# Kernel optimization log

Measured on AMD Instinct MI355X. Metric: run time of the kernel, lower is better.

The kernel has to match this reference:

```python
import jax, jax.numpy as jnp
import numpy as np

N = 100000   # num_nodes
E = 1250000  # num_edges
IN = 64
HID = 64
OUT = 64
LN_EPS = 1e-5


def _gcn_conv(x, src, dst, W, b, n):
    # PyG GCNConv: add self-loops, symmetric deg^{-1/2} normalization, then linear.
    h = x @ W  # (N, out)
    deg = jax.ops.segment_sum(jnp.ones(src.shape[0], h.dtype), dst, num_segments=n) + 1.0  # +1 self-loop
    dinv = jax.lax.rsqrt(deg)
    norm = dinv[src] * dinv[dst]  # (E,)
    out = jax.ops.segment_sum(h[src] * norm[:, None], dst, num_segments=n)
    out = out + h * (dinv * dinv)[:, None]  # self-loop message
    return out + b


def _sage_conv(x, src, dst, Wl, bl, Wr, n):
    # PyG SAGEConv(aggr='mean'): lin_l(mean_{j in N(i)} x_j) + lin_r(x_i); bias only in lin_l.
    cnt = jax.ops.segment_sum(jnp.ones(src.shape[0], x.dtype), dst, num_segments=n)
    agg = jax.ops.segment_sum(x[src], dst, num_segments=n) / jnp.maximum(cnt, 1.0)[:, None]
    return agg @ Wl + bl + x @ Wr


def _layer_norm(x, g, b):
    mu = jnp.mean(x, axis=-1, keepdims=True)
    var = jnp.var(x, axis=-1, keepdims=True)
    return (x - mu) * jax.lax.rsqrt(var + LN_EPS) * g + b


def setup_inputs() -> dict:
    key = jax.random.key(0)
    ks = jax.random.split(key, 16)
    def w(k, shape):
        fan_in = shape[0]
        return (jax.random.normal(k, shape, jnp.float32) / np.sqrt(fan_in)).astype(jnp.float32)
    x = jax.random.normal(ks[0], (N, IN), jnp.float32)
    edge_index = jax.random.randint(ks[1], (2, E), 0, N, dtype=jnp.int64)
    return {
        "x": x,
        "edge_index": edge_index,
        "gcn_w1": w(ks[2], (IN, HID)), "gcn_b1": jnp.zeros((HID,), jnp.float32),
        "gcn_w2": w(ks[3], (HID, OUT)), "gcn_b2": jnp.zeros((OUT,), jnp.float32),
        "sage_wl1": w(ks[4], (IN, HID)), "sage_bl1": jnp.zeros((HID,), jnp.float32),
        "sage_wr1": w(ks[5], (IN, HID)),
        "sage_wl2": w(ks[6], (HID, OUT)), "sage_bl2": jnp.zeros((OUT,), jnp.float32),
        "sage_wr2": w(ks[7], (HID, OUT)),
        "gcn_ln_g": jnp.ones((OUT,), jnp.float32), "gcn_ln_b": jnp.zeros((OUT,), jnp.float32),
        "sage_ln_g": jnp.ones((OUT,), jnp.float32), "sage_ln_b": jnp.zeros((OUT,), jnp.float32),
        "proj_w": w(ks[8], (2 * OUT, OUT)), "proj_b": jnp.zeros((OUT,), jnp.float32),
    }


def reference(x, edge_index, gcn_w1, gcn_b1, gcn_w2, gcn_b2,
              sage_wl1, sage_bl1, sage_wr1, sage_wl2, sage_bl2, sage_wr2,
              gcn_ln_g, gcn_ln_b, sage_ln_g, sage_ln_b, proj_w, proj_b):
    src, dst = edge_index[0], edge_index[1]
    n = x.shape[0]
    # GCN branch (dropout p=0 / eval -> identity)
    g = jax.nn.relu(_gcn_conv(x, src, dst, gcn_w1, gcn_b1, n))
    g = _gcn_conv(g, src, dst, gcn_w2, gcn_b2, n)
    # SAGE branch
    s = jax.nn.relu(_sage_conv(x, src, dst, sage_wl1, sage_bl1, sage_wr1, n))
    s = _sage_conv(s, src, dst, sage_wl2, sage_bl2, sage_wr2, n)
    # Norm + projected-concat fusion
    g = _layer_norm(g, gcn_ln_g, gcn_ln_b)
    s = _layer_norm(s, sage_ln_g, sage_ln_b)
    cat = jnp.concatenate([g, s], axis=-1)  # (N, 2*OUT)
    return cat @ proj_w + proj_b
```

## Files before the change

### kernel.cpp

```cpp
#include <hip/hip_runtime.h>


#define SCAN_CHUNK 2048

typedef __attribute__((ext_vector_type(8))) short short8;
typedef __attribute__((ext_vector_type(4))) short short4v;
typedef __attribute__((ext_vector_type(4))) float floatx4;

__device__ __forceinline__ unsigned short f2bf(float f) {
    unsigned int u = __float_as_uint(f);
    unsigned int r = u + 0x7FFFu + ((u >> 16) & 1u);
    return (unsigned short)(r >> 16);
}
__device__ __forceinline__ float bf2f(unsigned short h) {
    return __uint_as_float(((unsigned int)h) << 16);
}

__device__ __forceinline__ unsigned lds_addr(const void* p) {
    return (unsigned)(unsigned long long)(__attribute__((address_space(3))) const char*)p;
}

__device__ __forceinline__ short8 cat44(short4v lo, short4v hi) {
    short8 r;
    r[0] = lo[0]; r[1] = lo[1]; r[2] = lo[2]; r[3] = lo[3];
    r[4] = hi[0]; r[5] = hi[1]; r[6] = hi[2]; r[7] = hi[3];
    return r;
}

template<int NF, int CTB>
__device__ __forceinline__ void tr_read4(unsigned a0, short8 bf[4]) {
    short4v l0, h0, l1, h1, l2, h2, l3, h3;
    asm volatile(
        "ds_read_b64_tr_b16 %0, %8 offset:%9\n\t"
        "ds_read_b64_tr_b16 %1, %8 offset:%10\n\t"
        "ds_read_b64_tr_b16 %2, %8 offset:%11\n\t"
        "ds_read_b64_tr_b16 %3, %8 offset:%12\n\t"
        "ds_read_b64_tr_b16 %4, %8 offset:%13\n\t"
        "ds_read_b64_tr_b16 %5, %8 offset:%14\n\t"
        "ds_read_b64_tr_b16 %6, %8 offset:%15\n\t"
        "ds_read_b64_tr_b16 %7, %8 offset:%16\n\t"
        "s_waitcnt lgkmcnt(0)"
        : "=&v"(l0), "=&v"(h0), "=&v"(l1), "=&v"(h1),
          "=&v"(l2), "=&v"(h2), "=&v"(l3), "=&v"(h3)
        : "v"(a0),
          "i"((0 * NF + CTB + 0) * 128), "i"((1 * NF + CTB + 0) * 128),
          "i"((0 * NF + CTB + 1) * 128), "i"((1 * NF + CTB + 1) * 128),
          "i"((0 * NF + CTB + 2) * 128), "i"((1 * NF + CTB + 2) * 128),
          "i"((0 * NF + CTB + 3) * 128), "i"((1 * NF + CTB + 3) * 128)
        : "memory");
    bf[0] = cat44(l0, h0);
    bf[1] = cat44(l1, h1);
    bf[2] = cat44(l2, h2);
    bf[3] = cat44(l3, h3);
}

__global__ void k_count(const int* __restrict__ ei, int E, int* __restrict__ cnt,
                        int* __restrict__ rank) {
    int i = blockIdx.x * blockDim.x + threadIdx.x;
    int e = i * 4;
    if (e + 4 <= E) {
        int4 d = *(const int4*)&ei[E + e];
        int4 r;
        r.x = atomicAdd(&cnt[d.x], 1);
        r.y = atomicAdd(&cnt[d.y], 1);
        r.z = atomicAdd(&cnt[d.z], 1);
        r.w = atomicAdd(&cnt[d.w], 1);
        *(int4*)&rank[e] = r;
    } else {
        for (int j = e; j < E; ++j) rank[j] = atomicAdd(&cnt[ei[E + j]], 1);
    }
}

__global__ void k_scan_reduce(const int* __restrict__ cnt, int N, int* __restrict__ blockSums) {
    __shared__ int lds[256];
    int base = blockIdx.x * SCAN_CHUNK;
    int t = threadIdx.x;
    int s = 0;
    for (int j = 0; j < 8; ++j) {
        int idx = base + t * 8 + j;
        if (idx < N) s += cnt[idx];
    }
    lds[t] = s;
    __syncthreads();
    for (int d = 128; d > 0; d >>= 1) {
        if (t < d) lds[t] += lds[t + d];
        __syncthreads();
    }
    if (t == 0) blockSums[blockIdx.x] = lds[0];
}

__global__ void k_scan_spine(int* __restrict__ blockSums, int B) {
    if (threadIdx.x == 0 && blockIdx.x == 0) {
        int run = 0;
        for (int b = 0; b < B; ++b) { int v = blockSums[b]; blockSums[b] = run; run += v; }
    }
}

__global__ void k_scan_write(const int* __restrict__ cnt, int N,
                             const int* __restrict__ blockSums,
                             int* __restrict__ offs, float* __restrict__ dinv) {
    __shared__ int lds[256];
    int base = blockIdx.x * SCAN_CHUNK;
    int t = threadIdx.x;
    int v[8];
    int s = 0;
    for (int j = 0; j < 8; ++j) {
        int idx = base + t * 8 + j;
        v[j] = (idx < N) ? cnt[idx] : 0;
        s += v[j];
    }
    lds[t] = s;
    __syncthreads();
    for (int d = 1; d < 256; d <<= 1) {
        int x = (t >= d) ? lds[t - d] : 0;
        __syncthreads();
        lds[t] += x;
        __syncthreads();
    }
    int excl = (t == 0) ? 0 : lds[t - 1];
    int run = blockSums[blockIdx.x] + excl;
    for (int j = 0; j < 8; ++j) {
        int idx = base + t * 8 + j;
        if (idx < N) {
            offs[idx] = run;
            run += v[j];
            dinv[idx] = rsqrtf((float)v[j] + 1.0f);
            if (idx == N - 1) offs[N] = run;
        }
    }
}

__global__ void k_fill(const int* __restrict__ ei, int E, const int* __restrict__ offs,
                       const int* __restrict__ rank, const float* __restrict__ dinv,
                       int* __restrict__ csr, unsigned int* __restrict__ pk, int use_pk) {
    int i = blockIdx.x * blockDim.x + threadIdx.x;
    int e = i * 4;
    if (e + 4 <= E) {
        int4 s = *(const int4*)&ei[e];
        int4 d = *(const int4*)&ei[E + e];
        int4 r = *(const int4*)&rank[e];
        int p0 = offs[d.x] + r.x, p1 = offs[d.y] + r.y;
        int p2 = offs[d.z] + r.z, p3 = offs[d.w] + r.w;
        csr[p0] = s.x; csr[p1] = s.y; csr[p2] = s.z; csr[p3] = s.w;
        if (use_pk) {
            pk[p0] = ((unsigned)(d.x & 15) << 16) | f2bf(dinv[s.x] * dinv[d.x]);
            pk[p1] = ((unsigned)(d.y & 15) << 16) | f2bf(dinv[s.y] * dinv[d.y]);
            pk[p2] = ((unsigned)(d.z & 15) << 16) | f2bf(dinv[s.z] * dinv[d.z]);
            pk[p3] = ((unsigned)(d.w & 15) << 16) | f2bf(dinv[s.w] * dinv[d.w]);
        }
    } else {
        for (int j = e; j < E; ++j) {
            int dd = ei[E + j];
            int p = offs[dd] + rank[j];
            csr[p] = ei[j];
            if (use_pk) pk[p] = ((unsigned)(dd & 15) << 16) | f2bf(dinv[ei[j]] * dinv[dd]);
        }
    }
}

__global__ void k_xtobf16(const float* __restrict__ x, unsigned short* __restrict__ xb, int total) {
    int i = blockIdx.x * blockDim.x + threadIdx.x;
    int e = i * 8;
    if (e + 8 <= total) {
        float4 a = *(const float4*)&x[e];
        float4 b = *(const float4*)&x[e + 4];
        short8 o;
        o[0] = (short)f2bf(a.x); o[1] = (short)f2bf(a.y);
        o[2] = (short)f2bf(a.z); o[3] = (short)f2bf(a.w);
        o[4] = (short)f2bf(b.x); o[5] = (short)f2bf(b.y);
        o[6] = (short)f2bf(b.z); o[7] = (short)f2bf(b.w);
        *(short8*)&xb[e] = o;
    } else {
        for (int j = e; j < total; ++j) xb[j] = f2bf(x[j]);
    }
}

template<int ROWSH>
__launch_bounds__(256)
__global__ void k_gatherM(const unsigned short* __restrict__ feat,
                          const int* __restrict__ csr,
                          const unsigned int* __restrict__ pk,
                          const int* __restrict__ offs, const int* __restrict__ cnt,
                          const float* __restrict__ dinv,
                          unsigned short* __restrict__ agg, int N) {
    constexpr int NF = ROWSH / 16;
    constexpr int LPR = ROWSH / 8;
    constexpr int EPP = 64 / LPR;
    constexpr int PASSES = 32 / EPP;

    __shared__ unsigned short sbuf[4 * 32 * ROWSH];

    const int lane = threadIdx.x & 63;
    const int wave = threadIdx.x >> 6;
    const int base = blockIdx.x * 64 + wave * 16;
    if (base >= N) return;

    unsigned short* wb = &sbuf[wave * 32 * ROWSH];
    const unsigned wboff = lds_addr(wb);
    const int q = lane >> 4;
    const int d16 = lane & 15;

    const int se = lane / LPR;
    const int sf = (lane % LPR) * 8;
    const int sf_sub = sf >> 4;
    const int sf_lo = sf & 15;

    const int elo = offs[base];
    const int ehi = offs[min(base + 16, N)];

    floatx4 accg[4], accs[4];
#pragma unroll
    for (int i = 0; i < 4; ++i) {
        accg[i] = floatx4{0.f, 0.f, 0.f, 0.f};
        accs[i] = floatx4{0.f, 0.f, 0.f, 0.f};
    }

    const unsigned a0 = wboff + (unsigned)(q * 2 * NF) * 128u + (unsigned)d16 * 8u;

    for (int k0 = elo; k0 < ehi; k0 += 32) {
        short8 stg[PASSES];
#pragma unroll
        for (int p = 0; p < PASSES; ++p) {
            int idx = k0 + p * EPP + se;
            int src = csr[idx < ehi ? idx : ehi - 1];
            stg[p] = *(const short8*)&feat[(size_t)src * ROWSH + sf];
        }
        int i0 = k0 + q * 8;
        short8 aG, aS;
#pragma unroll
        for (int j = 0; j < 8; ++j) {
            unsigned u = pk[i0 + j];
            bool ok = ((int)(u >> 16) == d16) && (i0 + j < ehi);
            aG[j] = ok ? (short)(u & 0xffffu) : (short)0;
            aS[j] = ok ? (short)0x3F80 : (short)0;
        }
#pragma unroll
        for (int p = 0; p < PASSES; ++p) {
            int e = p * EPP + se;
            int elem = ((e >> 2) * NF + sf_sub) * 64 + (e & 3) * 16 + sf_lo;
            *(short8*)&wb[elem] = stg[p];
        }
        asm volatile("s_waitcnt lgkmcnt(0)" ::: "memory");
        __builtin_amdgcn_sched_barrier(0);

        short8 bG[4];
        tr_read4<NF, 0>(a0, bG);
#pragma unroll
        for (int ct = 0; ct < 4; ++ct)
            accg[ct] = __builtin_amdgcn_mfma_f32_16x16x32_bf16(aG, bG[ct], accg[ct], 0, 0, 0);
        if constexpr (NF == 8) {
            short8 bS[4];
            tr_read4<NF, 4>(a0, bS);
#pragma unroll
            for (int ct = 0; ct < 4; ++ct)
                accs[ct] = __builtin_amdgcn_mfma_f32_16x16x32_bf16(aS, bS[ct], accs[ct], 0, 0, 0);
        } else {
#pragma unroll
            for (int ct = 0; ct < 4; ++ct)
                accs[ct] = __builtin_amdgcn_mfma_f32_16x16x32_bf16(aS, bG[ct], accs[ct], 0, 0, 0);
        }
    }

    {
        short8 stg[PASSES];
#pragma unroll
        for (int p = 0; p < PASSES; ++p) {
            int nd = base + p * EPP + se;
            if (nd >= N) nd = N - 1;
            stg[p] = *(const short8*)&feat[(size_t)nd * ROWSH + sf];
        }
        float ds = dinv[min(base + d16, N - 1)];
        unsigned short wself = f2bf(ds * ds);
        short8 aG;
#pragma unroll
        for (int j = 0; j < 8; ++j) {
            bool ok = ((q * 8 + j) == d16) && (base + d16 < N);
            aG[j] = ok ? (short)wself : (short)0;
        }
#pragma unroll
        for (int p = 0; p < PASSES; ++p) {
            int e = p * EPP + se;
            int elem = ((e >> 2) * NF + sf_sub) * 64 + (e & 3) * 16 + sf_lo;
            *(short8*)&wb[elem] = stg[p];
        }
        asm volatile("s_waitcnt lgkmcnt(0)" ::: "memory");
        __builtin_amdgcn_sched_barrier(0);
        short8 bG[4];
        tr_read4<NF, 0>(a0, bG);
#pragma unroll
        for (int ct = 0; ct < 4; ++ct)
            accg[ct] = __builtin_amdgcn_mfma_f32_16x16x32_bf16(aG, bG[ct], accg[ct], 0, 0, 0);
    }

#pragma unroll
    for (int r = 0; r < 4; ++r) {
        int node = base + q * 4 + r;
        if (node < N) {
            float rn = 1.0f / fmaxf((float)cnt[node], 1.0f);
#pragma unroll
            for (int ct = 0; ct < 4; ++ct) {
                agg[(size_t)node * 128 + ct * 16 + d16]      = f2bf(accg[ct][r]);
                agg[(size_t)node * 128 + 64 + ct * 16 + d16] = f2bf(accs[ct][r] * rn);
            }
        }
    }
}

__device__ __forceinline__ void xor_reduce8(float4& a, float4& b) {
    a.x += __shfl_xor(a.x, 16, 64); a.y += __shfl_xor(a.y, 16, 64);
    a.z += __shfl_xor(a.z, 16, 64); a.w += __shfl_xor(a.w, 16, 64);
    b.x += __shfl_xor(b.x, 16, 64); b.y += __shfl_xor(b.y, 16, 64);
    b.z += __shfl_xor(b.z, 16, 64); b.w += __shfl_xor(b.w, 16, 64);
    a.x += __shfl_xor(a.x, 32, 64); a.y += __shfl_xor(a.y, 32, 64);
    a.z += __shfl_xor(a.z, 32, 64); a.w += __shfl_xor(a.w, 32, 64);
    b.x += __shfl_xor(b.x, 32, 64); b.y += __shfl_xor(b.y, 32, 64);
    b.z += __shfl_xor(b.z, 32, 64); b.w += __shfl_xor(b.w, 32, 64);
}

__device__ __forceinline__ float red16(float v) {
    v += __shfl_xor(v, 1, 64);
    v += __shfl_xor(v, 2, 64);
    v += __shfl_xor(v, 4, 64);
    v += __shfl_xor(v, 8, 64);
    return v;
}

__global__ void k_gather1_f32(const float* __restrict__ x, const int* __restrict__ csr,
                              const int* __restrict__ offs, const int* __restrict__ cnt,
                              const float* __restrict__ dinv,
                              unsigned short* __restrict__ agg, int N) {
    int lane = threadIdx.x & 63;
    int wave = threadIdx.x >> 6;
    int node = blockIdx.x * 4 + wave;
    if (node >= N) return;
    int c = lane & 15, grp = lane >> 4;

    int st = offs[node];
    int cn = cnt[node];
    float di = dinv[node];

    float4 aA = {0.f, 0.f, 0.f, 0.f}, aB = {0.f, 0.f, 0.f, 0.f};
    for (int e = 0; e < cn; e += 8) {
        int i0 = e + grp, i1 = e + 4 + grp;
        float m0 = (i0 < cn) ? 1.f : 0.f;
        float m1 = (i1 < cn) ? 1.f : 0.f;
        int s0 = csr[st + (i0 < cn ? i0 : cn - 1)];
        int s1 = csr[st + (i1 < cn ? i1 : cn - 1)];
        float w0 = m0 * dinv[s0];
        float w1 = m1 * dinv[s1];
        float4 v0 = *(const float4*)&x[(size_t)s0 * 64 + 4 * c];
        float4 v1 = *(const float4*)&x[(size_t)s1 * 64 + 4 * c];
        aA.x += w0 * v0.x + w1 * v1.x; aA.y += w0 * v0.y + w1 * v1.y;
        aA.z += w0 * v0.z + w1 * v1.z; aA.w += w0 * v0.w + w1 * v1.w;
        aB.x += m0 * v0.x + m1 * v1.x; aB.y += m0 * v0.y + m1 * v1.y;
        aB.z += m0 * v0.z + m1 * v1.z; aB.w += m0 * v0.w + m1 * v1.w;
    }
    xor_reduce8(aA, aB);

    if (grp == 0) {
        float4 sq = *(const float4*)&x[(size_t)node * 64 + 4 * c];
        float d2 = di * di;
        ushort4 o;
        o.x = f2bf(di * aA.x + d2 * sq.x); o.y = f2bf(di * aA.y + d2 * sq.y);
        o.z = f2bf(di * aA.z + d2 * sq.z); o.w = f2bf(di * aA.w + d2 * sq.w);
        *(ushort4*)&agg[(size_t)node * 128 + 4 * c] = o;
    } else if (grp == 1) {
        float rn = 1.0f / fmaxf((float)cn, 1.0f);
        ushort4 o;
        o.x = f2bf(aB.x * rn); o.y = f2bf(aB.y * rn);
        o.z = f2bf(aB.z * rn); o.w = f2bf(aB.w * rn);
        *(ushort4*)&agg[(size_t)node * 128 + 64 + 4 * c] = o;
    }
}

__global__ void k_gather2(const unsigned short* __restrict__ gs, const int* __restrict__ csr,
                          const int* __restrict__ offs, const int* __restrict__ cnt,
                          const float* __restrict__ dinv,
                          unsigned short* __restrict__ agg, int N) {
    int lane = threadIdx.x & 63;
    int wave = threadIdx.x >> 6;
    int node = blockIdx.x * 4 + wave;
    if (node >= N) return;
    int c = lane & 15, grp = lane >> 4;

    int st = offs[node];
    int cn = cnt[node];
    float di = dinv[node];

    float4 aC = {0.f, 0.f, 0.f, 0.f}, aD = {0.f, 0.f, 0.f, 0.f};
    for (int e = 0; e < cn; e += 8) {
        int i0 = e + grp, i1 = e + 4 + grp;
        float m0 = (i0 < cn) ? 1.f : 0.f;
        float m1 = (i1 < cn) ? 1.f : 0.f;
        int s0 = csr[st + (i0 < cn ? i0 : cn - 1)];
        int s1 = csr[st + (i1 < cn ? i1 : cn - 1)];
        float w0 = m0 * dinv[s0];
        float w1 = m1 * dinv[s1];
        const unsigned short* p0 = gs + (size_t)s0 * 128 + 4 * c;
        const unsigned short* p1 = gs + (size_t)s1 * 128 + 4 * c;
        ushort4 g0u = *(const ushort4*)p0;
        ushort4 g1u = *(const ushort4*)p1;
        ushort4 t0u = *(const ushort4*)(p0 + 64);
        ushort4 t1u = *(const ushort4*)(p1 + 64);
        aC.x += w0 * bf2f(g0u.x) + w1 * bf2f(g1u.x);
        aC.y += w0 * bf2f(g0u.y) + w1 * bf2f(g1u.y);
        aC.z += w0 * bf2f(g0u.z) + w1 * bf2f(g1u.z);
        aC.w += w0 * bf2f(g0u.w) + w1 * bf2f(g1u.w);
        aD.x += m0 * bf2f(t0u.x) + m1 * bf2f(t1u.x);
        aD.y += m0 * bf2f(t0u.y) + m1 * bf2f(t1u.y);
        aD.z += m0 * bf2f(t0u.z) + m1 * bf2f(t1u.z);
        aD.w += m0 * bf2f(t0u.w) + m1 * bf2f(t1u.w);
    }
    xor_reduce8(aC, aD);

    if (grp == 0) {
        ushort4 su = *(const ushort4*)&gs[(size_t)node * 128 + 4 * c];
        float d2 = di * di;
        ushort4 o;
        o.x = f2bf(di * aC.x + d2 * bf2f(su.x));
        o.y = f2bf(di * aC.y + d2 * bf2f(su.y));
        o.z = f2bf(di * aC.z + d2 * bf2f(su.z));
        o.w = f2bf(di * aC.w + d2 * bf2f(su.w));
        *(ushort4*)&agg[(size_t)node * 128 + 4 * c] = o;
    } else if (grp == 1) {
        float rn = 1.0f / fmaxf((float)cn, 1.0f);
        ushort4 o;
        o.x = f2bf(aD.x * rn); o.y = f2bf(aD.y * rn);
        o.z = f2bf(aD.z * rn); o.w = f2bf(aD.w * rn);
        *(ushort4*)&agg[(size_t)node * 128 + 64 + 4 * c] = o;
    }
}

__launch_bounds__(512, 1)
__global__ void k_gemm1(const unsigned short* __restrict__ agg,
                        const unsigned short* __restrict__ xb,
                        const float* __restrict__ xf, int use_xb,
                        const float* __restrict__ W1, const float* __restrict__ b1,
                        const float* __restrict__ Wl1, const float* __restrict__ bl1,
                        const float* __restrict__ Wr1,
                        unsigned short* __restrict__ buf1, int N) {
    alignas(16) __shared__ unsigned short sW[3][4096];
    int t = threadIdx.x;
    for (int i = t; i < 1536; i += 512) {
        int m = i >> 9;
        int rem = i & 511;
        int f = rem >> 6;
        int L = rem & 63;
        int kb = (f >> 2) * 32 + (L >> 4) * 8;
        int o = (f & 3) * 16 + (L & 15);
        const float* Wsrc = (m == 0) ? W1 : (m == 1) ? Wl1 : Wr1;
        unsigned short* dst = &sW[m][f * 512 + L * 8];
        #pragma unroll
        for (int j = 0; j < 8; ++j) dst[j] = f2bf(Wsrc[(kb + j) * 64 + o]);
    }
    __syncthreads();

    int lane = t & 63;
    int wave = t >> 6;
    int quad = lane >> 4;
    int n16 = lane & 15;
    int base = blockIdx.x * 128 + wave * 16;
    if (base >= N) return;

    int nm = base + n16;
    if (nm >= N) nm = N - 1;
    const unsigned short* ar = agg + (size_t)nm * 128;

    {
        short8 a0 = *(const short8*)(ar + quad * 8);
        short8 a1 = *(const short8*)(ar + 32 + quad * 8);
        floatx4 g0 = {0.f, 0.f, 0.f, 0.f}, g1 = g0, g2 = g0, g3 = g0;
        g0 = __builtin_amdgcn_mfma_f32_16x16x32_bf16(a0, *(const short8*)&sW[0][0 * 512 + lane * 8], g0, 0, 0, 0);
        g0 = __builtin_amdgcn_mfma_f32_16x16x32_bf16(a1, *(const short8*)&sW[0][4 * 512 + lane * 8], g0, 0, 0, 0);
        g1 = __builtin_amdgcn_mfma_f32_16x16x32_bf16(a0, *(const short8*)&sW[0][1 * 512 + lane * 8], g1, 0, 0, 0);
        g1 = __builtin_amdgcn_mfma_f32_16x16x32_bf16(a1, *(const short8*)&sW[0][5 * 512 + lane * 8], g1, 0, 0, 0);
        g2 = __builtin_amdgcn_mfma_f32_16x16x32_bf16(a0, *(const short8*)&sW[0][2 * 512 + lane * 8], g2, 0, 0, 0);
        g2 = __builtin_amdgcn_mfma_f32_16x16x32_bf16(a1, *(const short8*)&sW[0][6 * 512 + lane * 8], g2, 0, 0, 0);
        g3 = __builtin_amdgcn_mfma_f32_16x16x32_bf16(a0, *(const short8*)&sW[0][3 * 512 + lane * 8], g3, 0, 0, 0);
        g3 = __builtin_amdgcn_mfma_f32_16x16x32_bf16(a1, *(const short8*)&sW[0][7 * 512 + lane * 8], g3, 0, 0, 0);
        floatx4 gt[4] = {g0, g1, g2, g3};
        #pragma unroll
        for (int nt = 0; nt < 4; ++nt) {
            float bg = b1[nt * 16 + n16];
            #pragma unroll
            for (int r = 0; r < 4; ++r) {
                int node = base + quad * 4 + r;
                if (node < N)
                    buf1[(size_t)node * 128 + nt * 16 + n16] = f2bf(fmaxf(gt[nt][r] + bg, 0.f));
            }
        }
    }

    {
        short8 a0 = *(const short8*)(ar + 64 + quad * 8);
        short8 a1 = *(const short8*)(ar + 96 + quad * 8);
        short8 ax0, ax1;
        if (use_xb) {
            ax0 = *(const short8*)&xb[(size_t)nm * 64 + quad * 8];
            ax1 = *(const short8*)&xb[(size_t)nm * 64 + 32 + quad * 8];
        } else {
            float4 xq0 = *(const float4*)&xf[(size_t)nm * 64 + quad * 8];
            float4 xq1 = *(const float4*)&xf[(size_t)nm * 64 + quad * 8 + 4];
            float4 xq2 = *(const float4*)&xf[(size_t)nm * 64 + 32 + quad * 8];
            float4 xq3 = *(const float4*)&xf[(size_t)nm * 64 + 32 + quad * 8 + 4];
            ax0[0] = (short)f2bf(xq0.x); ax0[1] = (short)f2bf(xq0.y);
            ax0[2] = (short)f2bf(xq0.z); ax0[3] = (short)f2bf(xq0.w);
            ax0[4] = (short)f2bf(xq1.x); ax0[5] = (short)f2bf(xq1.y);
            ax0[6] = (short)f2bf(xq1.z); ax0[7] = (short)f2bf(xq1.w);
            ax1[0] = (short)f2bf(xq2.x); ax1[1] = (short)f2bf(xq2.y);
            ax1[2] = (short)f2bf(xq2.z); ax1[3] = (short)f2bf(xq2.w);
            ax1[4] = (short)f2bf(xq3.x); ax1[5] = (short)f2bf(xq3.y);
            ax1[6] = (short)f2bf(xq3.z); ax1[7] = (short)f2bf(xq3.w);
        }

        floatx4 s0 = {0.f, 0.f, 0.f, 0.f}, s1 = s0, s2 = s0, s3 = s0;
        s0 = __builtin_amdgcn_mfma_f32_16x16x32_bf16(a0, *(const short8*)&sW[1][0 * 512 + lane * 8], s0, 0, 0, 0);
        s0 = __builtin_amdgcn_mfma_f32_16x16x32_bf16(a1, *(const short8*)&sW[1][4 * 512 + lane * 8], s0, 0, 0, 0);
        s0 = __builtin_amdgcn_mfma_f32_16x16x32_bf16(ax0, *(const short8*)&sW[2][0 * 512 + lane * 8], s0, 0, 0, 0);
        s0 = __builtin_amdgcn_mfma_f32_16x16x32_bf16(ax1, *(const short8*)&sW[2][4 * 512 + lane * 8], s0, 0, 0, 0);
        s1 = __builtin_amdgcn_mfma_f32_16x16x32_bf16(a0, *(const short8*)&sW[1][1 * 512 + lane * 8], s1, 0, 0, 0);
        s1 = __builtin_amdgcn_mfma_f32_16x16x32_bf16(a1, *(const short8*)&sW[1][5 * 512 + lane * 8], s1, 0, 0, 0);
        s1 = __builtin_amdgcn_mfma_f32_16x16x32_bf16(ax0, *(const short8*)&sW[2][1 * 512 + lane * 8], s1, 0, 0, 0);
        s1 = __builtin_amdgcn_mfma_f32_16x16x32_bf16(ax1, *(const short8*)&sW[2][5 * 512 + lane * 8], s1, 0, 0, 0);
        s2 = __builtin_amdgcn_mfma_f32_16x16x32_bf16(a0, *(const short8*)&sW[1][2 * 512 + lane * 8], s2, 0, 0, 0);
        s2 = __builtin_amdgcn_mfma_f32_16x16x32_bf16(a1, *(const short8*)&sW[1][6 * 512 + lane * 8], s2, 0, 0, 0);
        s2 = __builtin_amdgcn_mfma_f32_16x16x32_bf16(ax0, *(const short8*)&sW[2][2 * 512 + lane * 8], s2, 0, 0, 0);
        s2 = __builtin_amdgcn_mfma_f32_16x16x32_bf16(ax1, *(const short8*)&sW[2][6 * 512 + lane * 8], s2, 0, 0, 0);
        s3 = __builtin_amdgcn_mfma_f32_16x16x32_bf16(a0, *(const short8*)&sW[1][3 * 512 + lane * 8], s3, 0, 0, 0);
        s3 = __builtin_amdgcn_mfma_f32_16x16x32_bf16(a1, *(const short8*)&sW[1][7 * 512 + lane * 8], s3, 0, 0, 0);
        s3 = __builtin_amdgcn_mfma_f32_16x16x32_bf16(ax0, *(const short8*)&sW[2][3 * 512 + lane * 8], s3, 0, 0, 0);
        s3 = __builtin_amdgcn_mfma_f32_16x16x32_bf16(ax1, *(const short8*)&sW[2][7 * 512 + lane * 8], s3, 0, 0, 0);
        floatx4 stl[4] = {s0, s1, s2, s3};
        #pragma unroll
        for (int nt = 0; nt < 4; ++nt) {
            float bs = bl1[nt * 16 + n16];
            #pragma unroll
            for (int r = 0; r < 4; ++r) {
                int node = base + quad * 4 + r;
                if (node < N)
                    buf1[(size_t)node * 128 + 64 + nt * 16 + n16] = f2bf(fmaxf(stl[nt][r] + bs, 0.f));
            }
        }
    }
}

__launch_bounds__(512, 1)
__global__ void k_gemm2(const unsigned short* __restrict__ agg,
                        const unsigned short* __restrict__ buf1,
                        const float* __restrict__ W2, const float* __restrict__ b2,
                        const float* __restrict__ Wl2, const float* __restrict__ bl2,
                        const float* __restrict__ Wr2,
                        const float* __restrict__ lngG, const float* __restrict__ lnbG,
                        const float* __restrict__ lngS, const float* __restrict__ lnbS,
                        const float* __restrict__ Pw, const float* __restrict__ Pb,
                        float* __restrict__ out, int N) {
    alignas(16) __shared__ unsigned short sW[3][4096];
    alignas(16) __shared__ unsigned short sP[8192];
    alignas(16) __shared__ unsigned short sT[8][16 * 132];
    int t = threadIdx.x;
    for (int i = t; i < 1536; i += 512) {
        int m = i >> 9;
        int rem = i & 511;
        int f = rem >> 6;
        int L = rem & 63;
        int kb = (f >> 2) * 32 + (L >> 4) * 8;
        int o = (f & 3) * 16 + (L & 15);
        const float* Wsrc = (m == 0) ? W2 : (m == 1) ? Wl2 : Wr2;
        unsigned short* dst = &sW[m][f * 512 + L * 8];
        #pragma unroll
        for (int j = 0; j < 8; ++j) dst[j] = f2bf(Wsrc[(kb + j) * 64 + o]);
    }
    for (int i = t; i < 1024; i += 512) {
        int f = i >> 6;
        int L = i & 63;
        int kb = (f >> 2) * 32 + (L >> 4) * 8;
        int o = (f & 3) * 16 + (L & 15);
        unsigned short* dst = &sP[f * 512 + L * 8];
        #pragma unroll
        for (int j = 0; j < 8; ++j) dst[j] = f2bf(Pw[(kb + j) * 64 + o]);
    }
    __syncthreads();

    int lane = t & 63;
    int wave = t >> 6;
    int quad = lane >> 4;
    int n16 = lane & 15;
    int base = blockIdx.x * 128 + wave * 16;
    if (base >= N) return;
    int nm = base + n16;
    if (nm >= N) nm = N - 1;
    const unsigned short* ar = agg + (size_t)nm * 128;
    const unsigned short* br = buf1 + (size_t)nm * 128;
    unsigned short* tw = &sT[wave][0];

    {
        short8 a0 = *(const short8*)(ar + quad * 8);
        short8 a1 = *(const short8*)(ar + 32 + quad * 8);
        floatx4 c0 = {0.f, 0.f, 0.f, 0.f}, c1 = c0, c2 = c0, c3 = c0;
        c0 = __builtin_amdgcn_mfma_f32_16x16x32_bf16(a0, *(const short8*)&sW[0][0 * 512 + lane * 8], c0, 0, 0, 0);
        c0 = __builtin_amdgcn_mfma_f32_16x16x32_bf16(a1, *(const short8*)&sW[0][4 * 512 + lane * 8], c0, 0, 0, 0);
        c1 = __builtin_amdgcn_mfma_f32_16x16x32_bf16(a0, *(const short8*)&sW[0][1 * 512 + lane * 8], c1, 0, 0, 0);
        c1 = __builtin_amdgcn_mfma_f32_16x16x32_bf16(a1, *(const short8*)&sW[0][5 * 512 + lane * 8], c1, 0, 0, 0);
        c2 = __builtin_amdgcn_mfma_f32_16x16x32_bf16(a0, *(const short8*)&sW[0][2 * 512 + lane * 8], c2, 0, 0, 0);
        c2 = __builtin_amdgcn_mfma_f32_16x16x32_bf16(a1, *(const short8*)&sW[0][6 * 512 + lane * 8], c2, 0, 0, 0);
        c3 = __builtin_amdgcn_mfma_f32_16x16x32_bf16(a0, *(const short8*)&sW[0][3 * 512 + lane * 8], c3, 0, 0, 0);
        c3 = __builtin_amdgcn_mfma_f32_16x16x32_bf16(a1, *(const short8*)&sW[0][7 * 512 + lane * 8], c3, 0, 0, 0);

        float bv0 = b2[n16], bv1 = b2[16 + n16], bv2 = b2[32 + n16], bv3 = b2[48 + n16];
        float gv0 = lngG[n16], gv1 = lngG[16 + n16], gv2 = lngG[32 + n16], gv3 = lngG[48 + n16];
        float ev0 = lnbG[n16], ev1 = lnbG[16 + n16], ev2 = lnbG[32 + n16], ev3 = lnbG[48 + n16];
        #pragma unroll
        for (int r = 0; r < 4; ++r) {
            float z0 = c0[r] + bv0, z1 = c1[r] + bv1, z2 = c2[r] + bv2, z3 = c3[r] + bv3;
            float s = red16(z0 + z1 + z2 + z3);
            float q = red16(z0 * z0 + z1 * z1 + z2 * z2 + z3 * z3);
            float mu = s * (1.0f / 64.0f);
            float var = fmaxf(q * (1.0f / 64.0f) - mu * mu, 0.0f);
            float rs = rsqrtf(var + 1e-5f);
            unsigned short* row = tw + (quad * 4 + r) * 132;
            row[n16]      = f2bf((z0 - mu) * rs * gv0 + ev0);
            row[16 + n16] = f2bf((z1 - mu) * rs * gv1 + ev1);
            row[32 + n16] = f2bf((z2 - mu) * rs * gv2 + ev2);
            row[48 + n16] = f2bf((z3 - mu) * rs * gv3 + ev3);
        }
    }

    {
        short8 a0 = *(const short8*)(ar + 64 + quad * 8);
        short8 a1 = *(const short8*)(ar + 96 + quad * 8);
        short8 v0 = *(const short8*)(br + 64 + quad * 8);
        short8 v1 = *(const short8*)(br + 96 + quad * 8);
        floatx4 c0 = {0.f, 0.f, 0.f, 0.f}, c1 = c0, c2 = c0, c3 = c0;
        c0 = __builtin_amdgcn_mfma_f32_16x16x32_bf16(a0, *(const short8*)&sW[1][0 * 512 + lane * 8], c0, 0, 0, 0);
        c0 = __builtin_amdgcn_mfma_f32_16x16x32_bf16(a1, *(const short8*)&sW[1][4 * 512 + lane * 8], c0, 0, 0, 0);
        c0 = __builtin_amdgcn_mfma_f32_16x16x32_bf16(v0, *(const short8*)&sW[2][0 * 512 + lane * 8], c0, 0, 0, 0);
        c0 = __builtin_amdgcn_mfma_f32_16x16x32_bf16(v1, *(const short8*)&sW[2][4 * 512 + lane * 8], c0, 0, 0, 0);
        c1 = __builtin_amdgcn_mfma_f32_16x16x32_bf16(a0, *(const short8*)&sW[1][1 * 512 + lane * 8], c1, 0, 0, 0);
        c1 = __builtin_amdgcn_mfma_f32_16x16x32_bf16(a1, *(const short8*)&sW[1][5 * 512 + lane * 8], c1, 0, 0, 0);
        c1 = __builtin_amdgcn_mfma_f32_16x16x32_bf16(v0, *(const short8*)&sW[2][1 * 512 + lane * 8], c1, 0, 0, 0);
        c1 = __builtin_amdgcn_mfma_f32_16x16x32_bf16(v1, *(const short8*)&sW[2][5 * 512 + lane * 8], c1, 0, 0, 0);
        c2 = __builtin_amdgcn_mfma_f32_16x16x32_bf16(a0, *(const short8*)&sW[1][2 * 512 + lane * 8], c2, 0, 0, 0);
        c2 = __builtin_amdgcn_mfma_f32_16x16x32_bf16(a1, *(const short8*)&sW[1][6 * 512 + lane * 8], c2, 0, 0, 0);
        c2 = __builtin_amdgcn_mfma_f32_16x16x32_bf16(v0, *(const short8*)&sW[2][2 * 512 + lane * 8], c2, 0, 0, 0);
        c2 = __builtin_amdgcn_mfma_f32_16x16x32_bf16(v1, *(const short8*)&sW[2][6 * 512 + lane * 8], c2, 0, 0, 0);
        c3 = __builtin_amdgcn_mfma_f32_16x16x32_bf16(a0, *(const short8*)&sW[1][3 * 512 + lane * 8], c3, 0, 0, 0);
        c3 = __builtin_amdgcn_mfma_f32_16x16x32_bf16(a1, *(const short8*)&sW[1][7 * 512 + lane * 8], c3, 0, 0, 0);
        c3 = __builtin_amdgcn_mfma_f32_16x16x32_bf16(v0, *(const short8*)&sW[2][3 * 512 + lane * 8], c3, 0, 0, 0);
        c3 = __builtin_amdgcn_mfma_f32_16x16x32_bf16(v1, *(const short8*)&sW[2][7 * 512 + lane * 8], c3, 0, 0, 0);

        float bv0 = bl2[n16], bv1 = bl2[16 + n16], bv2 = bl2[32 + n16], bv3 = bl2[48 + n16];
        float gv0 = lngS[n16], gv1 = lngS[16 + n16], gv2 = lngS[32 + n16], gv3 = lngS[48 + n16];
        float ev0 = lnbS[n16], ev1 = lnbS[16 + n16], ev2 = lnbS[32 + n16], ev3 = lnbS[48 + n16];
        #pragma unroll
        for (int r = 0; r < 4; ++r) {
            float z0 = c0[r] + bv0, z1 = c1[r] + bv1, z2 = c2[r] + bv2, z3 = c3[r] + bv3;
            float s = red16(z0 + z1 + z2 + z3);
            float q = red16(z0 * z0 + z1 * z1 + z2 * z2 + z3 * z3);
            float mu = s * (1.0f / 64.0f);
            float var = fmaxf(q * (1.0f / 64.0f) - mu * mu, 0.0f);
            float rs = rsqrtf(var + 1e-5f);
            unsigned short* row = tw + (quad * 4 + r) * 132 + 64;
            row[n16]      = f2bf((z0 - mu) * rs * gv0 + ev0);
            row[16 + n16] = f2bf((z1 - mu) * rs * gv1 + ev1);
            row[32 + n16] = f2bf((z2 - mu) * rs * gv2 + ev2);
            row[48 + n16] = f2bf((z3 - mu) * rs * gv3 + ev3);
        }
    }

    floatx4 o0 = {0.f, 0.f, 0.f, 0.f}, o1 = o0, o2 = o0, o3 = o0;
    #pragma unroll
    for (int ks = 0; ks < 4; ++ks) {
        const unsigned short* ap = tw + n16 * 132 + ks * 32 + quad * 8;
        short4v lo = *(const short4v*)ap;
        short4v hi = *(const short4v*)(ap + 4);
        short8 af;
        af[0] = lo[0]; af[1] = lo[1]; af[2] = lo[2]; af[3] = lo[3];
        af[4] = hi[0]; af[5] = hi[1]; af[6] = hi[2]; af[7] = hi[3];
        o0 = __builtin_amdgcn_mfma_f32_16x16x32_bf16(af, *(const short8*)&sP[(ks * 4 + 0) * 512 + lane * 8], o0, 0, 0, 0);
        o1 = __builtin_amdgcn_mfma_f32_16x16x32_bf16(af, *(const short8*)&sP[(ks * 4 + 1) * 512 + lane * 8], o1, 0, 0, 0);
        o2 = __builtin_amdgcn_mfma_f32_16x16x32_bf16(af, *(const short8*)&sP[(ks * 4 + 2) * 512 + lane * 8], o2, 0, 0, 0);
        o3 = __builtin_amdgcn_mfma_f32_16x16x32_bf16(af, *(const short8*)&sP[(ks * 4 + 3) * 512 + lane * 8], o3, 0, 0, 0);
    }
    float p0 = Pb[n16], p1 = Pb[16 + n16], p2 = Pb[32 + n16], p3 = Pb[48 + n16];
    floatx4 ot[4] = {o0, o1, o2, o3};
    float pv[4] = {p0, p1, p2, p3};
    #pragma unroll
    for (int nt = 0; nt < 4; ++nt) {
        #pragma unroll
        for (int r = 0; r < 4; ++r) {
            int node = base + quad * 4 + r;
            if (node < N) out[(size_t)node * 64 + nt * 16 + n16] = ot[nt][r] + pv[nt];
        }
    }
}

extern "C" void kernel_launch(void* const* d_in, const int* in_sizes, int n_in,
                              void* d_out, int out_size, void* d_ws, size_t ws_size,
                              hipStream_t stream) {
    const float* x        = (const float*)d_in[0];
    const int*   ei       = (const int*)d_in[1];
    const float* gcn_w1   = (const float*)d_in[2];
    const float* gcn_b1   = (const float*)d_in[3];
    const float* gcn_w2   = (const float*)d_in[4];
    const float* gcn_b2   = (const float*)d_in[5];
    const float* sage_wl1 = (const float*)d_in[6];
    const float* sage_bl1 = (const float*)d_in[7];
    const float* sage_wr1 = (const float*)d_in[8];
    const float* sage_wl2 = (const float*)d_in[9];
    const float* sage_bl2 = (const float*)d_in[10];
    const float* sage_wr2 = (const float*)d_in[11];
    const float* gcn_ln_g = (const float*)d_in[12];
    const float* gcn_ln_b = (const float*)d_in[13];
    const float* sage_ln_g = (const float*)d_in[14];
    const float* sage_ln_b = (const float*)d_in[15];
    const float* proj_w   = (const float*)d_in[16];
    const float* proj_b   = (const float*)d_in[17];
    float* out = (float*)d_out;

    const int N = in_sizes[0] / 64;
    const int E = in_sizes[1] / 2;
    const int B = (N + SCAN_CHUNK - 1) / SCAN_CHUNK;

    char* w = (char*)d_ws;
    size_t off = 0;
    auto alloc = [&](size_t bytes) -> void* {
        void* p = w + off;
        off = (off + bytes + 255) & ~(size_t)255;
        return p;
    };
    int*            cnt       = (int*)alloc((size_t)N * 4);
    int*            offs      = (int*)alloc((size_t)(N + 1) * 4);
    float*          dinv      = (float*)alloc((size_t)N * 4);
    int*            blockSums = (int*)alloc((size_t)(B + 1) * 4);
    int*            csr       = (int*)alloc((size_t)(E + 32) * 4);
    unsigned short* agg       = (unsigned short*)alloc((size_t)N * 128 * 2);
    unsigned short* buf1      = (unsigned short*)alloc((size_t)N * 128 * 2);
    size_t off_nonew = off;
    unsigned int*   pk        = (unsigned int*)alloc((size_t)(E + 32) * 4);
    unsigned short* xb        = (unsigned short*)alloc((size_t)N * 64 * 2);
    int use_new = (off <= ws_size) ? 1 : 0;
    if (!use_new) off = off_nonew;
    int* rank = (int*)agg;
    (void)n_in; (void)out_size;

    hipMemsetAsync(cnt, 0, (size_t)N * 4, stream);

    int e4Blocks = ((E + 3) / 4 + 255) / 256;
    k_count<<<e4Blocks, 256, 0, stream>>>(ei, E, cnt, rank);
    k_scan_reduce<<<B, 256, 0, stream>>>(cnt, N, blockSums);
    k_scan_spine<<<1, 64, 0, stream>>>(blockSums, B);
    k_scan_write<<<B, 256, 0, stream>>>(cnt, N, blockSums, offs, dinv);
    k_fill<<<e4Blocks, 256, 0, stream>>>(ei, E, offs, rank, dinv, csr, pk, use_new);

    if (use_new) {
        int xBlocks = ((N * 64 + 7) / 8 + 255) / 256;
        k_xtobf16<<<xBlocks, 256, 0, stream>>>(x, xb, N * 64);
        k_gatherM<64><<<(N + 63) / 64, 256, 0, stream>>>(xb, csr, pk, offs, cnt, dinv, agg, N);
        k_gemm1<<<(N + 127) / 128, 512, 0, stream>>>(agg, xb, x, 1, gcn_w1, gcn_b1,
                                                     sage_wl1, sage_bl1, sage_wr1, buf1, N);
        k_gatherM<128><<<(N + 63) / 64, 256, 0, stream>>>(buf1, csr, pk, offs, cnt, dinv, agg, N);
    } else {
        k_gather1_f32<<<(N + 3) / 4, 256, 0, stream>>>(x, csr, offs, cnt, dinv, agg, N);
        k_gemm1<<<(N + 127) / 128, 512, 0, stream>>>(agg, xb, x, 0, gcn_w1, gcn_b1,
                                                     sage_wl1, sage_bl1, sage_wr1, buf1, N);
        k_gather2<<<(N + 3) / 4, 256, 0, stream>>>(buf1, csr, offs, cnt, dinv, agg, N);
    }
    k_gemm2<<<(N + 127) / 128, 512, 0, stream>>>(agg, buf1, gcn_w2, gcn_b2,
                                                 sage_wl2, sage_bl2, sage_wr2,
                                                 gcn_ln_g, gcn_ln_b, sage_ln_g, sage_ln_b,
                                                 proj_w, proj_b, out, N);
}
```

Baseline: 342.0 us.

## Fold self-loops into CSR and double-buffer gather loads in k_gatherM

The scan now reserves one extra CSR slot per node. A new k_self kernel fills that slot with the node itself and its dinv² weight, flagged so the SAGE mean ignores it; this removes the separate self-loop epilogue in the gather kernel. The gather loop is restructured into a two-stage software pipeline: each lane loads one csr and pk entry per 32-edge chunk and broadcasts them with shuffles, and the feature loads for the next chunk are issued before the current one is processed. The LDS staging layout is also changed to a lane-linear write. This adds one small kernel, more registers and E+N-sized index arrays, and the fallback path now sees offsets that include self slots it never fills.

```diff
diff --git a/kernel.cpp b/kernel.cpp
--- a/kernel.cpp
+++ b/kernel.cpp
@@ -78,7 +78,7 @@
     int s = 0;
     for (int j = 0; j < 8; ++j) {
         int idx = base + t * 8 + j;
-        if (idx < N) s += cnt[idx];
+        if (idx < N) s += cnt[idx] + 1;
     }
     lds[t] = s;
     __syncthreads();
@@ -107,7 +107,7 @@
     for (int j = 0; j < 8; ++j) {
         int idx = base + t * 8 + j;
         v[j] = (idx < N) ? cnt[idx] : 0;
-        s += v[j];
+        s += (idx < N) ? v[j] + 1 : 0;
     }
     lds[t] = s;
     __syncthreads();
@@ -123,7 +123,7 @@
         int idx = base + t * 8 + j;
         if (idx < N) {
             offs[idx] = run;
-            run += v[j];
+            run += v[j] + 1;
             dinv[idx] = rsqrtf((float)v[j] + 1.0f);
             if (idx == N - 1) offs[N] = run;
         }
@@ -158,6 +158,18 @@
     }
 }
 
+__global__ void k_self(const int* __restrict__ offs, const int* __restrict__ cnt,
+                       const float* __restrict__ dinv,
+                       int* __restrict__ csr, unsigned int* __restrict__ pk, int N) {
+    int i = blockIdx.x * blockDim.x + threadIdx.x;
+    if (i < N) {
+        int pos = offs[i] + cnt[i];
+        float di = dinv[i];
+        csr[pos] = i;
+        pk[pos] = ((unsigned)(i & 15) << 16) | (1u << 20) | f2bf(di * di);
+    }
+}
+
 __global__ void k_xtobf16(const float* __restrict__ x, unsigned short* __restrict__ xb, int total) {
     int i = blockIdx.x * blockDim.x + threadIdx.x;
     int e = i * 8;
@@ -181,11 +193,9 @@
                           const int* __restrict__ csr,
                           const unsigned int* __restrict__ pk,
                           const int* __restrict__ offs, const int* __restrict__ cnt,
-                          const float* __restrict__ dinv,
                           unsigned short* __restrict__ agg, int N) {
     constexpr int NF = ROWSH / 16;
-    constexpr int LPR = ROWSH / 8;
-    constexpr int EPP = 64 / LPR;
+    constexpr int EPP = (NF == 8) ? 4 : 8;
     constexpr int PASSES = 32 / EPP;
 
     __shared__ unsigned short sbuf[4 * 32 * ROWSH];
@@ -200,10 +210,12 @@
     const int q = lane >> 4;
     const int d16 = lane & 15;
 
-    const int se = lane / LPR;
-    const int sf = (lane % LPR) * 8;
-    const int sf_sub = sf >> 4;
-    const int sf_lo = sf & 15;
+    const int parity = lane & 1;
+    const int ei_low = (lane >> 1) & 3;
+    const int sf_sub = (lane >> 3) & (NF - 1);
+    const int ei_high = (NF == 8) ? 0 : (lane >> 5);
+    const int ei = ei_high * 4 + ei_low;
+    const int sf = sf_sub * 16 + parity * 8;
 
     const int elo = offs[base];
     const int ehi = offs[min(base + 16, N)];
@@ -217,79 +229,78 @@
 
     const unsigned a0 = wboff + (unsigned)(q * 2 * NF) * 128u + (unsigned)d16 * 8u;
 
-    for (int k0 = elo; k0 < ehi; k0 += 32) {
-        short8 stg[PASSES];
-#pragma unroll
-        for (int p = 0; p < PASSES; ++p) {
-            int idx = k0 + p * EPP + se;
-            int src = csr[idx < ehi ? idx : ehi - 1];
-            stg[p] = *(const short8*)&feat[(size_t)src * ROWSH + sf];
-        }
-        int i0 = k0 + q * 8;
-        short8 aG, aS;
-#pragma unroll
-        for (int j = 0; j < 8; ++j) {
-            unsigned u = pk[i0 + j];
-            bool ok = ((int)(u >> 16) == d16) && (i0 + j < ehi);
-            aG[j] = ok ? (short)(u & 0xffffu) : (short)0;
-            aS[j] = ok ? (short)0x3F80 : (short)0;
-        }
-#pragma unroll
-        for (int p = 0; p < PASSES; ++p) {
-            int e = p * EPP + se;
-            int elem = ((e >> 2) * NF + sf_sub) * 64 + (e & 3) * 16 + sf_lo;
-            *(short8*)&wb[elem] = stg[p];
-        }
-        asm volatile("s_waitcnt lgkmcnt(0)" ::: "memory");
-        __builtin_amdgcn_sched_barrier(0);
-
-        short8 bG[4];
-        tr_read4<NF, 0>(a0, bG);
-#pragma unroll
-        for (int ct = 0; ct < 4; ++ct)
-            accg[ct] = __builtin_amdgcn_mfma_f32_16x16x32_bf16(aG, bG[ct], accg[ct], 0, 0, 0);
-        if constexpr (NF == 8) {
-            short8 bS[4];
-            tr_read4<NF, 4>(a0, bS);
+    if (elo < ehi) {
+        const int emax = ehi - 1;
+
+        auto meta = [&](int k0, int& csrv, unsigned& pkv) {
+            int idx = k0 + lane;
+            int idc = idx <= emax ? idx : emax;
+            csrv = csr[idc];
+            pkv = (idx < ehi) ? pk[idx] : 0x00100000u;
+        };
+        auto issue = [&](short8* stg, int csrv) {
+#pragma unroll
+            for (int p = 0; p < PASSES; ++p) {
+                int src = __shfl(csrv, p * EPP + ei, 64);
+                stg[p] = *(const short8*)&feat[(size_t)src * ROWSH + sf];
+            }
+        };
+        auto process = [&](const short8* stg, unsigned pkv) {
+#pragma unroll
+            for (int p = 0; p < PASSES; ++p)
+                *(short8*)&wb[p * 512 + lane * 8] = stg[p];
+            short8 aG, aS;
+#pragma unroll
+            for (int j = 0; j < 8; ++j) {
+                unsigned u = (unsigned)__shfl((int)pkv, q * 8 + j, 64);
+                unsigned hi = u >> 16;
+                bool match = (int)(hi & 15u) == d16;
+                aG[j] = match ? (short)(u & 0xFFFFu) : (short)0;
+                aS[j] = (match && !(hi & 16u)) ? (short)0x3F80 : (short)0;
+            }
+            asm volatile("s_waitcnt lgkmcnt(0)" ::: "memory");
+            __builtin_amdgcn_sched_barrier(0);
+            short8 bG[4];
+            tr_read4<NF, 0>(a0, bG);
 #pragma unroll
             for (int ct = 0; ct < 4; ++ct)
-                accs[ct] = __builtin_amdgcn_mfma_f32_16x16x32_bf16(aS, bS[ct], accs[ct], 0, 0, 0);
-        } else {
-#pragma unroll
-            for (int ct = 0; ct < 4; ++ct)
-                accs[ct] = __builtin_amdgcn_mfma_f32_16x16x32_bf16(aS, bG[ct], accs[ct], 0, 0, 0);
-        }
-    }
-
-    {
-        short8 stg[PASSES];
-#pragma unroll
-        for (int p = 0; p < PASSES; ++p) {
-            int nd = base + p * EPP + se;
-            if (nd >= N) nd = N - 1;
-            stg[p] = *(const short8*)&feat[(size_t)nd * ROWSH + sf];
-        }
-        float ds = dinv[min(base + d16, N - 1)];
-        unsigned short wself = f2bf(ds * ds);
-        short8 aG;
-#pragma unroll
-        for (int j = 0; j < 8; ++j) {
-            bool ok = ((q * 8 + j) == d16) && (base + d16 < N);
-            aG[j] = ok ? (short)wself : (short)0;
-        }
-#pragma unroll
-        for (int p = 0; p < PASSES; ++p) {
-            int e = p * EPP + se;
-            int elem = ((e >> 2) * NF + sf_sub) * 64 + (e & 3) * 16 + sf_lo;
-            *(short8*)&wb[elem] = stg[p];
-        }
-        asm volatile("s_waitcnt lgkmcnt(0)" ::: "memory");
-        __builtin_amdgcn_sched_barrier(0);
-        short8 bG[4];
-        tr_read4<NF, 0>(a0, bG);
-#pragma unroll
-        for (int ct = 0; ct < 4; ++ct)
-            accg[ct] = __builtin_amdgcn_mfma_f32_16x16x32_bf16(aG, bG[ct], accg[ct], 0, 0, 0);
+                accg[ct] = __builtin_amdgcn_mfma_f32_16x16x32_bf16(aG, bG[ct], accg[ct], 0, 0, 0);
+            if constexpr (NF == 8) {
+                short8 bS[4];
+                tr_read4<NF, 4>(a0, bS);
+#pragma unroll
+                for (int ct = 0; ct < 4; ++ct)
+                    accs[ct] = __builtin_amdgcn_mfma_f32_16x16x32_bf16(aS, bS[ct], accs[ct], 0, 0, 0);
+            } else {
+#pragma unroll
+                for (int ct = 0; ct < 4; ++ct)
+                    accs[ct] = __builtin_amdgcn_mfma_f32_16x16x32_bf16(aS, bG[ct], accs[ct], 0, 0, 0);
+            }
+        };
+
+        int csrvA, csrvN;
+        unsigned pkvA, pkvB, pkvN;
+        short8 sA[PASSES], sB[PASSES];
+
+        meta(elo, csrvA, pkvA);
+        issue(sA, csrvA);
+        meta(elo + 32, csrvN, pkvN);
+
+        int k0 = elo;
+        while (true) {
+            issue(sB, csrvN);
+            pkvB = pkvN;
+            meta(k0 + 64, csrvN, pkvN);
+            process(sA, pkvA);
+            k0 += 32;
+            if (k0 >= ehi) break;
+            issue(sA, csrvN);
+            pkvA = pkvN;
+            meta(k0 + 64, csrvN, pkvN);
+            process(sB, pkvB);
+            k0 += 32;
+            if (k0 >= ehi) break;
+        }
     }
 
 #pragma unroll
@@ -732,11 +743,11 @@
     int*            offs      = (int*)alloc((size_t)(N + 1) * 4);
     float*          dinv      = (float*)alloc((size_t)N * 4);
     int*            blockSums = (int*)alloc((size_t)(B + 1) * 4);
-    int*            csr       = (int*)alloc((size_t)(E + 32) * 4);
+    int*            csr       = (int*)alloc((size_t)(E + N + 64) * 4);
     unsigned short* agg       = (unsigned short*)alloc((size_t)N * 128 * 2);
     unsigned short* buf1      = (unsigned short*)alloc((size_t)N * 128 * 2);
     size_t off_nonew = off;
-    unsigned int*   pk        = (unsigned int*)alloc((size_t)(E + 32) * 4);
+    unsigned int*   pk        = (unsigned int*)alloc((size_t)(E + N + 64) * 4);
     unsigned short* xb        = (unsigned short*)alloc((size_t)N * 64 * 2);
     int use_new = (off <= ws_size) ? 1 : 0;
     if (!use_new) off = off_nonew;
@@ -753,12 +764,13 @@
     k_fill<<<e4Blocks, 256, 0, stream>>>(ei, E, offs, rank, dinv, csr, pk, use_new);
 
     if (use_new) {
+        k_self<<<(N + 255) / 256, 256, 0, stream>>>(offs, cnt, dinv, csr, pk, N);
         int xBlocks = ((N * 64 + 7) / 8 + 255) / 256;
         k_xtobf16<<<xBlocks, 256, 0, stream>>>(x, xb, N * 64);
-        k_gatherM<64><<<(N + 63) / 64, 256, 0, stream>>>(xb, csr, pk, offs, cnt, dinv, agg, N);
+        k_gatherM<64><<<(N + 63) / 64, 256, 0, stream>>>(xb, csr, pk, offs, cnt, agg, N);
         k_gemm1<<<(N + 127) / 128, 512, 0, stream>>>(agg, xb, x, 1, gcn_w1, gcn_b1,
                                                      sage_wl1, sage_bl1, sage_wr1, buf1, N);
-        k_gatherM<128><<<(N + 63) / 64, 256, 0, stream>>>(buf1, csr, pk, offs, cnt, dinv, agg, N);
+        k_gatherM<128><<<(N + 63) / 64, 256, 0, stream>>>(buf1, csr, pk, offs, cnt, agg, N);
     } else {
         k_gather1_f32<<<(N + 3) / 4, 256, 0, stream>>>(x, csr, offs, cnt, dinv, agg, N);
         k_gemm1<<<(N + 127) / 128, 512, 0, stream>>>(agg, xb, x, 0, gcn_w1, gcn_b1,
```

New measurement: 345.6 us. No clear change (+1.1%).
